# Optimization experiments

Measured on AMD Instinct MI355X. Metric: run time of the kernel, lower is better.

Reference implementation:

```python
import jax, jax.numpy as jnp
import numpy as np

B, N, F, K = 4096, 2048, 64, 64


def setup_inputs() -> dict:
    key = jax.random.key(0)
    k1, k2, k3, k4, k5 = jax.random.split(key, 5)
    X = jax.random.normal(k1, (B, N), dtype=jnp.float32)
    W = jax.random.normal(k2, (1, N), dtype=jnp.float32) * (1.0 / np.sqrt(N))
    b = jax.random.normal(k3, (1,), dtype=jnp.float32)
    vector = jax.random.normal(k4, (N, F, K), dtype=jnp.float32)
    feature2field = jax.random.randint(k5, (N,), 0, F, dtype=jnp.int32)
    return {"X": X, "W": W, "b": b, "vector": vector, "feature2field": feature2field}


def reference(X, W, b, vector, feature2field):
    # linear part: [B, 1]
    linear = X @ W.T + b
    # field-aware latent vector of feature i w.r.t. its own field: V[i] = vector[i, f2f[i]]  -> [N, K]
    V = vector[jnp.arange(vector.shape[0]), feature2field]
    # pairwise latent dot products S[i,j] = <V[i], V[j]>  -> [N, N]
    S = V @ V.T
    # Gram matrix over batch: P[i,j] = sum_b X[b,i] * X[b,j]  -> [N, N]
    P = X.T @ X
    # original loop accumulates sum over i<j and over batch of S[i,j] * X[:,i]*X[:,j],
    # then adds that scalar to every row of the linear output
    triu = jnp.triu(jnp.ones_like(S), k=1)
    interaction = jnp.sum(S * P * triu)
    return linear + interaction
```

## Files before the change

kernel.cpp:

```cpp
#include <hip/hip_runtime.h>

#define NB 4096
#define NN 2048
#define NF 64
#define NK 64
#define NCHUNK 32
#define NRG 16

#define WS_VG     0
#define WS_VNORM  (NN * NK)
#define WS_LIN    (WS_VNORM + NN)
#define WS_DD     (WS_LIN + NB)
#define WS_SROW   (WS_DD + NB)
#define WS_T      (WS_SROW + NB)

__global__ __launch_bounds__(256) void k_prep(const float* __restrict__ vec,
                                              const int* __restrict__ f2f,
                                              float* __restrict__ Vg,
                                              float* __restrict__ vnorm) {
    int i    = (blockIdx.x * 256 + threadIdx.x) >> 6;
    int lane = threadIdx.x & 63;
    int f = f2f[i];
    float v = vec[(size_t)i * (NF * NK) + (size_t)f * NK + lane];
    Vg[(size_t)i * NK + lane] = v;
    float sq = v * v;
    #pragma unroll
    for (int m = 32; m; m >>= 1) sq += __shfl_xor(sq, m, 64);
    if (lane == 0) vnorm[i] = sq;
}

template <bool PART>
__global__ __launch_bounds__(256) void k_main(const float* __restrict__ X,
                                              const float* __restrict__ Wg,
                                              const float* __restrict__ Vg,
                                              const float* __restrict__ vn,
                                              float* __restrict__ Tout,
                                              float* __restrict__ lin_ws,
                                              float* __restrict__ dd_ws) {
    __shared__ float sm[256 * 65];

    const int t  = threadIdx.x;
    const int rg = blockIdx.x >> 5;
    const int c  = blockIdx.x & 31;
    const int r0 = rg * 256;
    const int i0 = c * 64;

    {
        const int rr = t >> 4;
        const int c4 = (t & 15) * 4;
        #pragma unroll
        for (int m = 0; m < 16; ++m) {
            int r = rr + 16 * m;
            float4 x = *reinterpret_cast<const float4*>(
                X + (size_t)(r0 + r) * NN + i0 + c4);
            sm[(c4 + 0) * 257 + r] = x.x;
            sm[(c4 + 1) * 257 + r] = x.y;
            sm[(c4 + 2) * 257 + r] = x.z;
            sm[(c4 + 3) * 257 + r] = x.w;
        }
    }

    float acc[NK];
    #pragma unroll
    for (int k = 0; k < NK; ++k) acc[k] = 0.f;
    float lin = 0.f, dd = 0.f;

    const float* __restrict__ vbase = Vg + (size_t)i0 * NK;
    const float* __restrict__ wbase = Wg + i0;
    const float* __restrict__ nbase = vn + i0;

    __syncthreads();

    #pragma unroll 2
    for (int i = 0; i < 64; ++i) {
        float x  = sm[i * 257 + t];
        float wv = wbase[i];
        float nv = nbase[i];
        lin = fmaf(x, wv, lin);
        dd  = fmaf(x * x, nv, dd);
        #pragma unroll
        for (int k = 0; k < NK; ++k)
            acc[k] = fmaf(x, vbase[i * NK + k], acc[k]);
    }

    __syncthreads();
    #pragma unroll
    for (int k = 0; k < NK; ++k)
        sm[t * 65 + k] = acc[k];
    __syncthreads();

    {
        const int rr = t >> 4;
        const int k4 = (t & 15) * 4;
        #pragma unroll
        for (int m = 0; m < 16; ++m) {
            int r = rr + 16 * m;
            float4 v;
            v.x = sm[r * 65 + k4 + 0];
            v.y = sm[r * 65 + k4 + 1];
            v.z = sm[r * 65 + k4 + 2];
            v.w = sm[r * 65 + k4 + 3];
            if (PART) {
                *reinterpret_cast<float4*>(
                    Tout + ((size_t)c * NB + r0 + r) * NK + k4) = v;
            } else {
                float* p = Tout + (size_t)(r0 + r) * NK + k4;
                atomicAdd(p + 0, v.x); atomicAdd(p + 1, v.y);
                atomicAdd(p + 2, v.z); atomicAdd(p + 3, v.w);
            }
        }
    }
    atomicAdd(&lin_ws[r0 + t], lin);
    atomicAdd(&dd_ws[r0 + t], dd);
}

template <int NCH>
__global__ __launch_bounds__(256) void k_red(const float* __restrict__ Tp,
                                             const float* __restrict__ dd_ws,
                                             float* __restrict__ srow) {
    int tid = blockIdx.x * 256 + threadIdx.x;
    int row = tid >> 4;
    int k4  = (tid & 15) * 4;
    float4 s = {0.f, 0.f, 0.f, 0.f};
    for (int c = 0; c < NCH; ++c) {
        float4 p = *reinterpret_cast<const float4*>(
            Tp + ((size_t)c * NB + row) * NK + k4);
        s.x += p.x; s.y += p.y; s.z += p.z; s.w += p.w;
    }
    float v = s.x * s.x + s.y * s.y + s.z * s.z + s.w * s.w;
    #pragma unroll
    for (int m = 1; m < 16; m <<= 1) v += __shfl_xor(v, m, 64);
    if ((threadIdx.x & 15) == 0) srow[row] = v - dd_ws[row];
}

__global__ __launch_bounds__(256) void k_final(const float* __restrict__ lin_ws,
                                               const float* __restrict__ srow,
                                               const float* __restrict__ bptr,
                                               float* __restrict__ out) {
    __shared__ double red[256];
    int t = threadIdx.x;
    double a = 0.0;
    for (int j = t; j < NB; j += 256) a += (double)srow[j];
    red[t] = a;
    __syncthreads();
    #pragma unroll
    for (int s = 128; s; s >>= 1) {
        if (t < s) red[t] += red[t + s];
        __syncthreads();
    }
    float inter = (float)(0.5 * red[0]);
    float bias  = bptr[0];
    for (int j = t; j < NB; j += 256) out[j] = lin_ws[j] + bias + inter;
}

extern "C" void kernel_launch(void* const* d_in, const int* in_sizes, int n_in,
                              void* d_out, int out_size, void* d_ws, size_t ws_size,
                              hipStream_t stream) {
    const float* X    = (const float*)d_in[0];
    const float* W    = (const float*)d_in[1];
    const float* bias = (const float*)d_in[2];
    const float* vec  = (const float*)d_in[3];
    const int*   f2f  = (const int*)d_in[4];
    float* out = (float*)d_out;

    float* ws    = (float*)d_ws;
    float* Vg    = ws + WS_VG;
    float* vnorm = ws + WS_VNORM;
    float* lin   = ws + WS_LIN;
    float* dd    = ws + WS_DD;
    float* srow  = ws + WS_SROW;
    float* T     = ws + WS_T;

    const size_t need_part = ((size_t)WS_T + (size_t)NCHUNK * NB * NK) * 4;
    const bool part = ws_size >= need_part;

    hipMemsetAsync(lin, 0, 2 * NB * sizeof(float), stream);
    if (!part)
        hipMemsetAsync(T, 0, (size_t)NB * NK * sizeof(float), stream);

    k_prep<<<512, 256, 0, stream>>>(vec, f2f, Vg, vnorm);
    if (part) {
        k_main<true><<<NRG * NCHUNK, 256, 0, stream>>>(X, W, Vg, vnorm, T, lin, dd);
        k_red<NCHUNK><<<NB * 16 / 256, 256, 0, stream>>>(T, dd, srow);
    } else {
        k_main<false><<<NRG * NCHUNK, 256, 0, stream>>>(X, W, Vg, vnorm, T, lin, dd);
        k_red<1><<<NB * 16 / 256, 256, 0, stream>>>(T, dd, srow);
    }
    k_final<<<1, 256, 0, stream>>>(lin, srow, bias, out);
}
```

Before: 136.4 us.

## Load X rows directly into registers and replace atomics with partial buffers

k_main no longer stages X through a transposed shared-memory tile. Each thread now loads its own 64-element X row slice as float4s straight into registers and writes its 64 partial T values with direct float4 stores, which removes the LDS traffic and the __syncthreads barriers. The lin/dd atomics and their memset are replaced by per-chunk partial arrays that k_red sums alongside T, and the fallback atomic path for a small workspace is removed. The trade-offs are per-thread strided global reads and writes (each thread touches a 256-byte span), which coalesce less well, more register pressure, and a hard requirement for the larger workspace.

```diff
diff --git a/kernel.cpp b/kernel.cpp
--- a/kernel.cpp
+++ b/kernel.cpp
@@ -4,15 +4,16 @@
 #define NN 2048
 #define NF 64
 #define NK 64
-#define NCHUNK 32
+#define NCH 32
 #define NRG 16
 
 #define WS_VG     0
-#define WS_VNORM  (NN * NK)
-#define WS_LIN    (WS_VNORM + NN)
-#define WS_DD     (WS_LIN + NB)
-#define WS_SROW   (WS_DD + NB)
-#define WS_T      (WS_SROW + NB)
+#define WS_VNORM  (WS_VG + NN * NK)
+#define WS_LINP   (WS_VNORM + NN)
+#define WS_DDP    (WS_LINP + NCH * NB)
+#define WS_SROW   (WS_DDP + NCH * NB)
+#define WS_LINT   (WS_SROW + NB)
+#define WS_T      (WS_LINT + NB)
 
 __global__ __launch_bounds__(256) void k_prep(const float* __restrict__ vec,
                                               const int* __restrict__ f2f,
@@ -29,111 +30,85 @@
     if (lane == 0) vnorm[i] = sq;
 }
 
-template <bool PART>
 __global__ __launch_bounds__(256) void k_main(const float* __restrict__ X,
                                               const float* __restrict__ Wg,
                                               const float* __restrict__ Vg,
                                               const float* __restrict__ vn,
-                                              float* __restrict__ Tout,
-                                              float* __restrict__ lin_ws,
-                                              float* __restrict__ dd_ws) {
-    __shared__ float sm[256 * 65];
+                                              float* __restrict__ Tp,
+                                              float* __restrict__ linp,
+                                              float* __restrict__ ddp) {
+    const int t   = threadIdx.x;
+    const int rg  = blockIdx.x >> 5;
+    const int c   = blockIdx.x & 31;
+    const int row = rg * 256 + t;
+    const int i0  = c * 64;
 
-    const int t  = threadIdx.x;
-    const int rg = blockIdx.x >> 5;
-    const int c  = blockIdx.x & 31;
-    const int r0 = rg * 256;
-    const int i0 = c * 64;
+    const float4* __restrict__ xr = reinterpret_cast<const float4*>(
+        X + (size_t)row * NN + i0);
+    const float* __restrict__ vb = Vg + (size_t)i0 * NK;
+    const float* __restrict__ wb = Wg + i0;
+    const float* __restrict__ nb = vn + i0;
 
-    {
-        const int rr = t >> 4;
-        const int c4 = (t & 15) * 4;
-        #pragma unroll
-        for (int m = 0; m < 16; ++m) {
-            int r = rr + 16 * m;
-            float4 x = *reinterpret_cast<const float4*>(
-                X + (size_t)(r0 + r) * NN + i0 + c4);
-            sm[(c4 + 0) * 257 + r] = x.x;
-            sm[(c4 + 1) * 257 + r] = x.y;
-            sm[(c4 + 2) * 257 + r] = x.z;
-            sm[(c4 + 3) * 257 + r] = x.w;
-        }
-    }
+    float4 xv[16];
+    #pragma unroll
+    for (int j = 0; j < 16; ++j) xv[j] = xr[j];
 
     float acc[NK];
     #pragma unroll
     for (int k = 0; k < NK; ++k) acc[k] = 0.f;
     float lin = 0.f, dd = 0.f;
 
-    const float* __restrict__ vbase = Vg + (size_t)i0 * NK;
-    const float* __restrict__ wbase = Wg + i0;
-    const float* __restrict__ nbase = vn + i0;
-
-    __syncthreads();
-
-    #pragma unroll 2
-    for (int i = 0; i < 64; ++i) {
-        float x  = sm[i * 257 + t];
-        float wv = wbase[i];
-        float nv = nbase[i];
-        lin = fmaf(x, wv, lin);
-        dd  = fmaf(x * x, nv, dd);
+    #pragma unroll
+    for (int j = 0; j < 16; ++j) {
+        float xs0 = xv[j].x, xs1 = xv[j].y, xs2 = xv[j].z, xs3 = xv[j].w;
         #pragma unroll
-        for (int k = 0; k < NK; ++k)
-            acc[k] = fmaf(x, vbase[i * NK + k], acc[k]);
+        for (int e = 0; e < 4; ++e) {
+            const int i = 4 * j + e;
+            float x = (e == 0) ? xs0 : (e == 1) ? xs1 : (e == 2) ? xs2 : xs3;
+            lin = fmaf(x, wb[i], lin);
+            dd  = fmaf(x * x, nb[i], dd);
+            #pragma unroll
+            for (int k = 0; k < NK; ++k)
+                acc[k] = fmaf(x, vb[i * NK + k], acc[k]);
+        }
     }
 
-    __syncthreads();
+    float4* out4 = reinterpret_cast<float4*>(Tp + ((size_t)c * NB + row) * NK);
     #pragma unroll
-    for (int k = 0; k < NK; ++k)
-        sm[t * 65 + k] = acc[k];
-    __syncthreads();
-
-    {
-        const int rr = t >> 4;
-        const int k4 = (t & 15) * 4;
-        #pragma unroll
-        for (int m = 0; m < 16; ++m) {
-            int r = rr + 16 * m;
-            float4 v;
-            v.x = sm[r * 65 + k4 + 0];
-            v.y = sm[r * 65 + k4 + 1];
-            v.z = sm[r * 65 + k4 + 2];
-            v.w = sm[r * 65 + k4 + 3];
-            if (PART) {
-                *reinterpret_cast<float4*>(
-                    Tout + ((size_t)c * NB + r0 + r) * NK + k4) = v;
-            } else {
-                float* p = Tout + (size_t)(r0 + r) * NK + k4;
-                atomicAdd(p + 0, v.x); atomicAdd(p + 1, v.y);
-                atomicAdd(p + 2, v.z); atomicAdd(p + 3, v.w);
-            }
-        }
-    }
-    atomicAdd(&lin_ws[r0 + t], lin);
-    atomicAdd(&dd_ws[r0 + t], dd);
+    for (int k4 = 0; k4 < 16; ++k4)
+        out4[k4] = make_float4(acc[4 * k4], acc[4 * k4 + 1],
+                               acc[4 * k4 + 2], acc[4 * k4 + 3]);
+    linp[c * NB + row] = lin;
+    ddp [c * NB + row] = dd;
 }
 
-template <int NCH>
 __global__ __launch_bounds__(256) void k_red(const float* __restrict__ Tp,
-                                             const float* __restrict__ dd_ws,
-                                             float* __restrict__ srow) {
-    int tid = blockIdx.x * 256 + threadIdx.x;
-    int row = tid >> 4;
-    int k4  = (tid & 15) * 4;
+                                             const float* __restrict__ linp,
+                                             const float* __restrict__ ddp,
+                                             float* __restrict__ srow,
+                                             float* __restrict__ lint) {
+    int gid = blockIdx.x * 256 + threadIdx.x;
+    int row = gid >> 4;
+    int g   = gid & 15;
     float4 s = {0.f, 0.f, 0.f, 0.f};
-    for (int c = 0; c < NCH; ++c) {
+    for (int cc = 0; cc < NCH; ++cc) {
         float4 p = *reinterpret_cast<const float4*>(
-            Tp + ((size_t)c * NB + row) * NK + k4);
+            Tp + ((size_t)cc * NB + row) * NK + g * 4);
         s.x += p.x; s.y += p.y; s.z += p.z; s.w += p.w;
     }
     float v = s.x * s.x + s.y * s.y + s.z * s.z + s.w * s.w;
+    float l = linp[g * NB + row] + linp[(g + 16) * NB + row];
+    float d = ddp [g * NB + row] + ddp [(g + 16) * NB + row];
     #pragma unroll
-    for (int m = 1; m < 16; m <<= 1) v += __shfl_xor(v, m, 64);
-    if ((threadIdx.x & 15) == 0) srow[row] = v - dd_ws[row];
+    for (int m = 1; m < 16; m <<= 1) {
+        v += __shfl_xor(v, m, 64);
+        l += __shfl_xor(l, m, 64);
+        d += __shfl_xor(d, m, 64);
+    }
+    if (g == 0) { srow[row] = v - d; lint[row] = l; }
 }
 
-__global__ __launch_bounds__(256) void k_final(const float* __restrict__ lin_ws,
+__global__ __launch_bounds__(256) void k_final(const float* __restrict__ lint,
                                                const float* __restrict__ srow,
                                                const float* __restrict__ bptr,
                                                float* __restrict__ out) {
@@ -150,7 +125,7 @@
     }
     float inter = (float)(0.5 * red[0]);
     float bias  = bptr[0];
-    for (int j = t; j < NB; j += 256) out[j] = lin_ws[j] + bias + inter;
+    for (int j = t; j < NB; j += 256) out[j] = lint[j] + bias + inter;
 }
 
 extern "C" void kernel_launch(void* const* d_in, const int* in_sizes, int n_in,
@@ -166,25 +141,14 @@
     float* ws    = (float*)d_ws;
     float* Vg    = ws + WS_VG;
     float* vnorm = ws + WS_VNORM;
-    float* lin   = ws + WS_LIN;
-    float* dd    = ws + WS_DD;
+    float* linp  = ws + WS_LINP;
+    float* ddp   = ws + WS_DDP;
     float* srow  = ws + WS_SROW;
-    float* T     = ws + WS_T;
-
-    const size_t need_part = ((size_t)WS_T + (size_t)NCHUNK * NB * NK) * 4;
-    const bool part = ws_size >= need_part;
-
-    hipMemsetAsync(lin, 0, 2 * NB * sizeof(float), stream);
-    if (!part)
-        hipMemsetAsync(T, 0, (size_t)NB * NK * sizeof(float), stream);
+    float* lint  = ws + WS_LINT;
+    float* Tp    = ws + WS_T;
 
     k_prep<<<512, 256, 0, stream>>>(vec, f2f, Vg, vnorm);
-    if (part) {
-        k_main<true><<<NRG * NCHUNK, 256, 0, stream>>>(X, W, Vg, vnorm, T, lin, dd);
-        k_red<NCHUNK><<<NB * 16 / 256, 256, 0, stream>>>(T, dd, srow);
-    } else {
-        k_main<false><<<NRG * NCHUNK, 256, 0, stream>>>(X, W, Vg, vnorm, T, lin, dd);
-        k_red<1><<<NB * 16 / 256, 256, 0, stream>>>(T, dd, srow);
-    }
-    k_final<<<1, 256, 0, stream>>>(lin, srow, bias, out);
+    k_main<<<NRG * NCH, 256, 0, stream>>>(X, W, Vg, vnorm, Tp, linp, ddp);
+    k_red<<<NB * 16 / 256, 256, 0, stream>>>(Tp, linp, ddp, srow, lint);
+    k_final<<<1, 256, 0, stream>>>(lint, srow, bias, out);
 }
```

Result: slower. 147.3 us (+8.0%).
